# Kernel tuning notes

Measured on AMD Instinct MI355X. Metric: run time of the kernel, lower is better.

The kernel has to match this reference:

```python
import jax, jax.numpy as jnp
import numpy as np

N = 4096          # number of bodies
DIM = 2           # 2D physics (Parallax robot soccer)
K_BROAD = 4 * N   # broad phase keeps first 4N AABB overlaps (per source)
K_EXACT = N       # exact phase keeps first N true penetrations (per source)


def setup_inputs() -> dict:
    key = jax.random.key(0)
    k1, k2 = jax.random.split(key)
    # disk bodies scattered in a ~160x160 arena -> dense enough for many hits
    pos = jax.random.normal(k1, (N, DIM), dtype=jnp.float32) * 40.0
    radius = jax.random.uniform(k2, (N,), dtype=jnp.float32, minval=0.5, maxval=1.5)
    return {"pos": pos, "radius": radius}


def _forward(pos, radius):
    n = pos.shape[0]
    # ---- broad phase: sphere AABB = pos +- radius; two boxes overlap iff
    # |p_i - p_j| <= r_i + r_j on every axis. Full O(N^2) scan (as in source),
    # compact the first K_BROAD hits in row-major (i*n + j) order.
    d = jnp.abs(pos[:, None, :] - pos[None, :, :])            # [N,N,DIM]
    rsum = radius[:, None] + radius[None, :]                  # [N,N]
    overlap = jnp.all(d <= rsum[..., None], axis=-1)          # [N,N] bool
    overlap = overlap & ~jnp.eye(n, dtype=bool)               # skip self-pairs
    flat = overlap.reshape(-1)                                # [N*N]
    rank = jnp.cumsum(flat.astype(jnp.int32)) - 1             # slot of each hit
    valid = flat & (rank < K_BROAD)
    slot = jnp.where(valid, rank, K_BROAD)                    # K_BROAD -> dropped
    ii = jnp.repeat(jnp.arange(n, dtype=jnp.int32), n)
    jj = jnp.tile(jnp.arange(n, dtype=jnp.int32), n)
    bi = jnp.full((K_BROAD,), -1, jnp.int32).at[slot].set(ii, mode='drop')
    bj = jnp.full((K_BROAD,), -1, jnp.int32).at[slot].set(jj, mode='drop')
    # ---- exact phase: sphere-sphere penetration test on broad pairs,
    # keep first K_EXACT real penetrations (gather-compute-compact).
    gi = jnp.clip(bi, 0, n - 1)
    gj = jnp.clip(bj, 0, n - 1)
    dv = pos[gi] - pos[gj]                                    # [K_BROAD,DIM]
    dist = jnp.sqrt(jnp.sum(dv * dv, axis=-1) + 1e-12)
    pen_depth = radius[gi] + radius[gj] - dist                # >0 means overlap
    hit = (bi >= 0) & (pen_depth > 0)
    erank = jnp.cumsum(hit.astype(jnp.int32)) - 1
    evalid = hit & (erank < K_EXACT)
    eslot = jnp.where(evalid, erank, K_EXACT)                 # K_EXACT -> dropped
    pen_vec = dv * (pen_depth / dist)[:, None]                # penetration vector
    ei = jnp.full((K_EXACT,), -1, jnp.int32).at[eslot].set(bi, mode='drop')
    ej = jnp.full((K_EXACT,), -1, jnp.int32).at[eslot].set(bj, mode='drop')
    ev = jnp.zeros((K_EXACT, pos.shape[-1]), pos.dtype).at[eslot].set(pen_vec, mode='drop')
    # ---- resolve: each body of the pair is pushed half the penetration apart,
    si = jnp.where(ei >= 0, ei, n)                            # n -> dropped
    sj = jnp.where(ej >= 0, ej, n)
    new_i = pos[jnp.clip(ei, 0, n - 1)] + 0.5 * ev
    new_j = pos[jnp.clip(ej, 0, n - 1)] - 0.5 * ev
    out = pos.at[si].set(new_i, mode='drop')
    out = out.at[sj].set(new_j, mode='drop')
    return out


def reference(pos, radius):
    return _forward(pos, radius)
```

## Files before the change

### kernel.cpp

```cpp
#include <hip/hip_runtime.h>

#define NB 4096
#define KBROAD (4 * NB)
#define KEXACT NB
typedef unsigned long long u64;

__global__ __launch_bounds__(256) void count_kernel(
    const float2* __restrict__ pos, const float* __restrict__ rad,
    int* __restrict__ row_counts, u64* __restrict__ masks,
    unsigned* __restrict__ hitbits, int* __restrict__ last_i,
    int* __restrict__ last_j) {
  int gid = blockIdx.x * blockDim.x + threadIdx.x;
  if (gid < 512) hitbits[gid] = 0;
  if (gid < NB) { last_i[gid] = -1; last_j[gid] = -1; }
  int wave = gid >> 6;
  int lane = gid & 63;
  int r0 = wave * 2;
  float2 p0 = pos[r0], p1 = pos[r0 + 1];
  float ra0 = rad[r0], ra1 = rad[r0 + 1];
  u64 mw0 = 0, mw1 = 0;
  int c0 = 0, c1 = 0;
  for (int c = 0; c < 64; ++c) {
    int j = c * 64 + lane;
    float2 pj = pos[j];
    float rj = rad[j];
    float rs0 = ra0 + rj, rs1 = ra1 + rj;
    bool h0 = (j != r0) && (fabsf(p0.x - pj.x) <= rs0) && (fabsf(p0.y - pj.y) <= rs0);
    bool h1 = (j != r0 + 1) && (fabsf(p1.x - pj.x) <= rs1) && (fabsf(p1.y - pj.y) <= rs1);
    u64 m0 = __ballot(h0);
    u64 m1 = __ballot(h1);
    if (lane == c) { mw0 = m0; mw1 = m1; }
    c0 += __popcll(m0);
    c1 += __popcll(m1);
  }
  masks[(size_t)r0 * 64 + lane] = mw0;
  masks[(size_t)(r0 + 1) * 64 + lane] = mw1;
  if (lane == 0) { row_counts[r0] = c0; row_counts[r0 + 1] = c1; }
}

__global__ __launch_bounds__(256) void fill_kernel(
    const float2* __restrict__ pos, const float* __restrict__ rad,
    const int* __restrict__ row_counts, const u64* __restrict__ masks,
    float2* __restrict__ penvec, unsigned* __restrict__ pij,
    unsigned* __restrict__ hitbits) {
  __shared__ int rb[NB];
  __shared__ int wsum[4];
  int t = threadIdx.x;
  int wv = t >> 6, lane = t & 63;
  int c[16], s = 0;
  #pragma unroll
  for (int k = 0; k < 16; ++k) { c[k] = row_counts[t * 16 + k]; s += c[k]; }
  int v = s;
  #pragma unroll
  for (int off = 1; off < 64; off <<= 1) {
    int u = __shfl_up(v, off);
    if (lane >= off) v += u;
  }
  if (lane == 63) wsum[wv] = v;
  __syncthreads();
  int wbase = 0;
  #pragma unroll
  for (int w = 0; w < 4; ++w) if (w < wv) wbase += wsum[w];
  int run = wbase + v - s;
  #pragma unroll
  for (int k = 0; k < 16; ++k) { rb[k * 256 + t] = run; run += c[k]; }
  __syncthreads();
  for (int q = 0; q < 4; ++q) {
    int r = blockIdx.x * 16 + wv * 4 + q;
    int rowbase = rb[(r & 15) * 256 + (r >> 4)];
    if (rowbase >= KBROAD) continue;
    u64 myw = masks[(size_t)r * 64 + lane];
    int cnt = __popcll(myw);
    int v2 = cnt;
    #pragma unroll
    for (int off = 1; off < 64; off <<= 1) {
      int u = __shfl_up(v2, off);
      if (lane >= off) v2 += u;
    }
    int rank = rowbase + v2 - cnt;
    if (!myw) continue;
    float2 pr = pos[r];
    float rr = rad[r];
    u64 m = myw;
    while (m && rank < KBROAD) {
      int b = __builtin_ctzll(m);
      m &= m - 1;
      int j = (lane << 6) + b;
      float2 pj = pos[j];
      float dx = pr.x - pj.x, dy = pr.y - pj.y;
      float ss = __fadd_rn(__fadd_rn(__fmul_rn(dx, dx), __fmul_rn(dy, dy)), 1e-12f);
      float dist = __fsqrt_rn(ss);
      float pen = __fsub_rn(__fadd_rn(rr, rad[j]), dist);
      if (pen > 0.0f) {
        float sc = __fdiv_rn(pen, dist);
        penvec[rank] = make_float2(__fmul_rn(dx, sc), __fmul_rn(dy, sc));
        pij[rank] = ((unsigned)r << 16) | (unsigned)j;
        atomicOr(&hitbits[rank >> 5], 1u << (rank & 31));
      }
      ++rank;
    }
  }
}

__global__ __launch_bounds__(256) void exact_kernel(
    const unsigned* __restrict__ hitbits, const unsigned* __restrict__ pij,
    const float2* __restrict__ penvec, float2* __restrict__ ev,
    int* __restrict__ last_i, int* __restrict__ last_j) {
  __shared__ unsigned hb[512];
  __shared__ int wb[512];
  __shared__ int wsum[4];
  int t = threadIdx.x;
  int wv = t >> 6, lane = t & 63;
  unsigned w0 = hitbits[2 * t], w1 = hitbits[2 * t + 1];
  hb[2 * t] = w0;
  hb[2 * t + 1] = w1;
  int cnt = __popc(w0) + __popc(w1);
  int v = cnt;
  #pragma unroll
  for (int off = 1; off < 64; off <<= 1) {
    int u = __shfl_up(v, off);
    if (lane >= off) v += u;
  }
  if (lane == 63) wsum[wv] = v;
  __syncthreads();
  int wbase = 0;
  #pragma unroll
  for (int w = 0; w < 4; ++w) if (w < wv) wbase += wsum[w];
  int excl = wbase + v - cnt;
  wb[2 * t] = excl;
  wb[2 * t + 1] = excl + __popc(w0);
  __syncthreads();
  int s = blockIdx.x * 256 + t;
  unsigned word = hb[s >> 5];
  if ((word >> (s & 31)) & 1u) {
    int rank = wb[s >> 5] + __popc(word & ((1u << (s & 31)) - 1u));
    if (rank < KEXACT) {
      ev[rank] = penvec[s];
      unsigned p = pij[s];
      atomicMax(&last_i[p >> 16], rank);
      atomicMax(&last_j[p & 0xFFFFu], rank);
    }
  }
}

__global__ __launch_bounds__(256) void combine_kernel(
    const float2* __restrict__ pos, const int* __restrict__ last_i,
    const int* __restrict__ last_j, const float2* __restrict__ ev,
    float2* __restrict__ out) {
  int b = blockIdx.x * blockDim.x + threadIdx.x;
  float2 p = pos[b];
  int lj = last_j[b], li = last_i[b];
  float2 o = p;
  if (lj >= 0) {
    o.x = __fsub_rn(p.x, __fmul_rn(0.5f, ev[lj].x));
    o.y = __fsub_rn(p.y, __fmul_rn(0.5f, ev[lj].y));
  } else if (li >= 0) {
    o.x = __fadd_rn(p.x, __fmul_rn(0.5f, ev[li].x));
    o.y = __fadd_rn(p.y, __fmul_rn(0.5f, ev[li].y));
  }
  out[b] = o;
}

extern "C" void kernel_launch(void* const* d_in, const int* in_sizes, int n_in,
                              void* d_out, int out_size, void* d_ws, size_t ws_size,
                              hipStream_t stream) {
  const float2* pos = (const float2*)d_in[0];
  const float* rad = (const float*)d_in[1];
  float2* out = (float2*)d_out;

  u64* masks = (u64*)d_ws;
  float2* penvec = (float2*)(masks + (size_t)NB * 64);
  float2* ev = penvec + KBROAD;
  int* row_counts = (int*)(ev + KEXACT);
  unsigned* pij = (unsigned*)(row_counts + NB);
  unsigned* hitbits = pij + KBROAD;
  int* last_i = (int*)(hitbits + 512);
  int* last_j = last_i + NB;

  count_kernel<<<512, 256, 0, stream>>>(pos, rad, row_counts, masks, hitbits,
                                        last_i, last_j);
  fill_kernel<<<256, 256, 0, stream>>>(pos, rad, row_counts, masks, penvec,
                                       pij, hitbits);
  exact_kernel<<<64, 256, 0, stream>>>(hitbits, pij, penvec, ev, last_i,
                                       last_j);
  combine_kernel<<<16, 256, 0, stream>>>(pos, last_i, last_j, ev, out);
}
```

Before: 96.59 us.

## Fuse exact compaction and resolve into one single-block kernel with shared state

Merges the exact-phase compaction and the combine step into one 1024-thread single-block kernel. last_i, last_j and ev now live in shared memory, which removes one launch and global atomics. Hit flags become a per-slot int array written by the fill kernel instead of atomicOr bitmasks, so the hitbits and last arrays no longer need zeroing in count_kernel. The trade-off is that all compaction runs on a single block (one CU), and the total is recomputed there from row_counts.

```diff
diff --git a/kernel.cpp b/kernel.cpp
--- a/kernel.cpp
+++ b/kernel.cpp
@@ -7,12 +7,8 @@
 
 __global__ __launch_bounds__(256) void count_kernel(
     const float2* __restrict__ pos, const float* __restrict__ rad,
-    int* __restrict__ row_counts, u64* __restrict__ masks,
-    unsigned* __restrict__ hitbits, int* __restrict__ last_i,
-    int* __restrict__ last_j) {
+    int* __restrict__ row_counts, u64* __restrict__ masks) {
   int gid = blockIdx.x * blockDim.x + threadIdx.x;
-  if (gid < 512) hitbits[gid] = 0;
-  if (gid < NB) { last_i[gid] = -1; last_j[gid] = -1; }
   int wave = gid >> 6;
   int lane = gid & 63;
   int r0 = wave * 2;
@@ -42,7 +38,7 @@
     const float2* __restrict__ pos, const float* __restrict__ rad,
     const int* __restrict__ row_counts, const u64* __restrict__ masks,
     float2* __restrict__ penvec, unsigned* __restrict__ pij,
-    unsigned* __restrict__ hitbits) {
+    int* __restrict__ hit) {
   __shared__ int rb[NB];
   __shared__ int wsum[4];
   int t = threadIdx.x;
@@ -91,74 +87,93 @@
       float ss = __fadd_rn(__fadd_rn(__fmul_rn(dx, dx), __fmul_rn(dy, dy)), 1e-12f);
       float dist = __fsqrt_rn(ss);
       float pen = __fsub_rn(__fadd_rn(rr, rad[j]), dist);
-      if (pen > 0.0f) {
+      int h = (pen > 0.0f) ? 1 : 0;
+      hit[rank] = h;
+      if (h) {
         float sc = __fdiv_rn(pen, dist);
         penvec[rank] = make_float2(__fmul_rn(dx, sc), __fmul_rn(dy, sc));
         pij[rank] = ((unsigned)r << 16) | (unsigned)j;
-        atomicOr(&hitbits[rank >> 5], 1u << (rank & 31));
       }
       ++rank;
     }
   }
 }
 
-__global__ __launch_bounds__(256) void exact_kernel(
-    const unsigned* __restrict__ hitbits, const unsigned* __restrict__ pij,
-    const float2* __restrict__ penvec, float2* __restrict__ ev,
-    int* __restrict__ last_i, int* __restrict__ last_j) {
-  __shared__ unsigned hb[512];
-  __shared__ int wb[512];
-  __shared__ int wsum[4];
+__global__ __launch_bounds__(1024) void final_kernel(
+    const float2* __restrict__ pos, const int* __restrict__ row_counts,
+    const int* __restrict__ hit, const unsigned* __restrict__ pij,
+    const float2* __restrict__ penvec, float2* __restrict__ out) {
+  __shared__ int last_i[NB];
+  __shared__ int last_j[NB];
+  __shared__ float2 ev[KEXACT];
+  __shared__ int wsum[16];
+  __shared__ int wscan[16];
   int t = threadIdx.x;
   int wv = t >> 6, lane = t & 63;
-  unsigned w0 = hitbits[2 * t], w1 = hitbits[2 * t + 1];
-  hb[2 * t] = w0;
-  hb[2 * t + 1] = w1;
-  int cnt = __popc(w0) + __popc(w1);
+  for (int b = t; b < NB; b += 1024) { last_i[b] = -1; last_j[b] = -1; }
+
+  int ps = row_counts[4 * t] + row_counts[4 * t + 1] +
+           row_counts[4 * t + 2] + row_counts[4 * t + 3];
+  #pragma unroll
+  for (int off = 32; off; off >>= 1) ps += __shfl_down(ps, off);
+  if (lane == 0) wsum[wv] = ps;
+  __syncthreads();
+  int total = 0;
+  #pragma unroll
+  for (int w = 0; w < 16; ++w) total += wsum[w];
+  if (total > KBROAD) total = KBROAD;
+
+  int base = t * 16;
+  int cnt = 0;
+  unsigned hm = 0;
+  #pragma unroll
+  for (int k = 0; k < 16; ++k) {
+    int s = base + k;
+    int h = (s < total) ? hit[s] : 0;
+    cnt += h;
+    hm |= (unsigned)h << k;
+  }
   int v = cnt;
   #pragma unroll
   for (int off = 1; off < 64; off <<= 1) {
     int u = __shfl_up(v, off);
     if (lane >= off) v += u;
   }
-  if (lane == 63) wsum[wv] = v;
+  if (lane == 63) wscan[wv] = v;
   __syncthreads();
   int wbase = 0;
   #pragma unroll
-  for (int w = 0; w < 4; ++w) if (w < wv) wbase += wsum[w];
-  int excl = wbase + v - cnt;
-  wb[2 * t] = excl;
-  wb[2 * t + 1] = excl + __popc(w0);
-  __syncthreads();
-  int s = blockIdx.x * 256 + t;
-  unsigned word = hb[s >> 5];
-  if ((word >> (s & 31)) & 1u) {
-    int rank = wb[s >> 5] + __popc(word & ((1u << (s & 31)) - 1u));
-    if (rank < KEXACT) {
-      ev[rank] = penvec[s];
-      unsigned p = pij[s];
-      atomicMax(&last_i[p >> 16], rank);
-      atomicMax(&last_j[p & 0xFFFFu], rank);
+  for (int w = 0; w < 16; ++w) if (w < wv) wbase += wscan[w];
+  int rank = wbase + v - cnt;
+
+  #pragma unroll
+  for (int k = 0; k < 16; ++k) {
+    if ((hm >> k) & 1u) {
+      if (rank < KEXACT) {
+        int s = base + k;
+        ev[rank] = penvec[s];
+        unsigned p = pij[s];
+        atomicMax(&last_i[p >> 16], rank);
+        atomicMax(&last_j[p & 0xFFFFu], rank);
+      }
+      ++rank;
     }
   }
-}
+  __syncthreads();
 
-__global__ __launch_bounds__(256) void combine_kernel(
-    const float2* __restrict__ pos, const int* __restrict__ last_i,
-    const int* __restrict__ last_j, const float2* __restrict__ ev,
-    float2* __restrict__ out) {
-  int b = blockIdx.x * blockDim.x + threadIdx.x;
-  float2 p = pos[b];
-  int lj = last_j[b], li = last_i[b];
-  float2 o = p;
-  if (lj >= 0) {
-    o.x = __fsub_rn(p.x, __fmul_rn(0.5f, ev[lj].x));
-    o.y = __fsub_rn(p.y, __fmul_rn(0.5f, ev[lj].y));
-  } else if (li >= 0) {
-    o.x = __fadd_rn(p.x, __fmul_rn(0.5f, ev[li].x));
-    o.y = __fadd_rn(p.y, __fmul_rn(0.5f, ev[li].y));
+  for (int b = t; b < NB; b += 1024) {
+    float2 p = pos[b];
+    int lj = last_j[b], li = last_i[b];
+    float2 o = p;
+    if (lj >= 0) {
+      o.x = __fsub_rn(p.x, __fmul_rn(0.5f, ev[lj].x));
+      o.y = __fsub_rn(p.y, __fmul_rn(0.5f, ev[lj].y));
+    } else if (li >= 0) {
+      o.x = __fadd_rn(p.x, __fmul_rn(0.5f, ev[li].x));
+      o.y = __fadd_rn(p.y, __fmul_rn(0.5f, ev[li].y));
+    }
+    out[b] = o;
   }
-  out[b] = o;
 }
 
 extern "C" void kernel_launch(void* const* d_in, const int* in_sizes, int n_in,
@@ -170,18 +185,12 @@
 
   u64* masks = (u64*)d_ws;
   float2* penvec = (float2*)(masks + (size_t)NB * 64);
-  float2* ev = penvec + KBROAD;
-  int* row_counts = (int*)(ev + KEXACT);
+  int* row_counts = (int*)(penvec + KBROAD);
   unsigned* pij = (unsigned*)(row_counts + NB);
-  unsigned* hitbits = pij + KBROAD;
-  int* last_i = (int*)(hitbits + 512);
-  int* last_j = last_i + NB;
+  int* hit = (int*)(pij + KBROAD);
 
-  count_kernel<<<512, 256, 0, stream>>>(pos, rad, row_counts, masks, hitbits,
-                                        last_i, last_j);
+  count_kernel<<<512, 256, 0, stream>>>(pos, rad, row_counts, masks);
   fill_kernel<<<256, 256, 0, stream>>>(pos, rad, row_counts, masks, penvec,
-                                       pij, hitbits);
-  exact_kernel<<<64, 256, 0, stream>>>(hitbits, pij, penvec, ev, last_i,
-                                       last_j);
-  combine_kernel<<<16, 256, 0, stream>>>(pos, last_i, last_j, ev, out);
+                                       pij, hit);
+  final_kernel<<<1, 1024, 0, stream>>>(pos, row_counts, hit, pij, penvec, out);
 }
```

Result: slower. 100.0 us (+3.5%).
